# Performance work log

Measured on AMD Instinct MI355X. Metric: run time of the kernel, lower is better.

## Reference

```python
import jax, jax.numpy as jnp
import numpy as np

B, D, K, P = 4096, 510, 128, 332


def setup_inputs() -> dict:
    key = jax.random.key(0)
    k0, k1, k2, k3, k4 = jax.random.split(key, 5)
    z = jax.random.normal(k0, (B, D), dtype=jnp.float32)
    z_pre = jax.random.normal(k1, (B, D), dtype=jnp.float32)
    codebook = jax.random.normal(k2, (K, D), dtype=jnp.float32)
    phrase_table = jax.random.normal(k3, (P, D), dtype=jnp.float32)
    position_number = jax.random.randint(k4, (B,), 0, P, dtype=jnp.int64)
    return {"z": z, "z_pre": z_pre, "codebook": codebook,
            "phrase_table": phrase_table, "position_number": position_number}


def _vq(z, codebook):
    # squared L2 distance via ||z||^2 + ||c||^2 - 2 z.c  (same argmin as tf.norm)
    d2 = (jnp.sum(z * z, axis=-1, keepdims=True)
          + jnp.sum(codebook * codebook, axis=-1)[None, :]
          - 2.0 * jnp.einsum('bd,kd->bk', z, codebook))  # [B, K]
    k = jnp.argmin(d2, axis=-1)                           # [B]
    return codebook[k]                                    # gather -> [B, D]


def reference(z, z_pre, codebook, phrase_table, position_number):
    z_q = _vq(z, codebook)
    z_pre_q = _vq(z_pre, codebook)
    phrase_emb = phrase_table[position_number]            # [B, D]
    combined = z_q + z_pre_q + phrase_emb                 # decoder input in original model
    return combined
```

## Files before the change

kernel.cpp:

```cpp
#include <hip/hip_runtime.h>


#define BHALF 4096
#define D 510
#define K_CODES 128
#define CHB 32768
#define NCHUNK 8
#define WS_NEED (512 + NCHUNK * CHB)

using f32x4  = __attribute__((ext_vector_type(4))) float;
using bf16x8 = __attribute__((ext_vector_type(8))) short;

__device__ __forceinline__ unsigned short f2bf(float f) {
    union { float f; unsigned int u; } v; v.f = f;
    return (unsigned short)((v.u + 0x7FFFu + ((v.u >> 16) & 1u)) >> 16);
}
__device__ __forceinline__ float bf2f(unsigned short h) {
    union { unsigned int u; float f; } v; v.u = ((unsigned int)h) << 16;
    return v.f;
}
__device__ __forceinline__ bool lexlt(float va, int ia, float vb, int ib) {
    return va < vb || (va == vb && ia < ib);
}
#define MFMA16 __builtin_amdgcn_mfma_f32_16x16x32_bf16

__global__ void prep_kernel(const float* __restrict__ cb,
                            float* __restrict__ cnorm,
                            char* __restrict__ img) {
    const int code = blockIdx.x;
    const int l = threadIdx.x;
    const int swz = (code & 7) << 4;
    float s = 0.f;
    #pragma unroll
    for (int i = 0; i < 8; ++i) {
        const int k = l + 64 * i;
        const float v = (k < D) ? cb[(size_t)code * D + k] : 0.f;
        s = fmaf(v, v, s);
        const unsigned short hi = f2bf(v);
        const unsigned short lo = f2bf(v - bf2f(hi));
        char* base = img + (size_t)(k >> 6) * CHB + code * 128;
        const int off = ((k & 63) * 2) ^ swz;
        *(unsigned short*)(base + off) = hi;
        *(unsigned short*)(base + 16384 + off) = lo;
    }
    #pragma unroll
    for (int m = 1; m < 64; m <<= 1) s += __shfl_xor(s, m, 64);
    if (l == 0) cnorm[code] = s;
}

__launch_bounds__(512, 1)
__global__ void main_kernel(const float* __restrict__ z,
                            const float* __restrict__ zp,
                            const float* __restrict__ cb,
                            const float* __restrict__ ph,
                            const int* __restrict__ pos,
                            const float* __restrict__ cnorm,
                            const char* __restrict__ img,
                            float* __restrict__ out) {
    __shared__ __align__(1024) char lds[131072];

    const int tid  = threadIdx.x;
    const int lane = tid & 63;
    const int wu   = __builtin_amdgcn_readfirstlane(tid >> 6);
    const int wn   = wu & 3;
    const int kh   = wu >> 2;
    const int l15  = lane & 15;
    const int kg16 = (lane >> 4) * 16;
    const int r0   = blockIdx.x * 16;

    #pragma unroll
    for (int i = 0; i < 8; ++i) {
        const int u = tid + 512 * i;
        const int row = u >> 7;
        const int col = (u & 127) * 4;
        const float* src = (row < 16) ? z + (size_t)(r0 + row) * D
                                      : zp + (size_t)(r0 + row - 16) * D;
        const float2 va = *(const float2*)(src + col);
        const float2 vb = (col + 2 < D) ? *(const float2*)(src + col + 2)
                                        : make_float2(0.f, 0.f);
        const unsigned short h0 = f2bf(va.x), h1 = f2bf(va.y),
                             h2 = f2bf(vb.x), h3 = f2bf(vb.y);
        const unsigned short g0 = f2bf(va.x - bf2f(h0)), g1 = f2bf(va.y - bf2f(h1)),
                             g2 = f2bf(vb.x - bf2f(h2)), g3 = f2bf(vb.y - bf2f(h3));
        uint2 hi2, lo2;
        hi2.x = (unsigned)h0 | ((unsigned)h1 << 16);
        hi2.y = (unsigned)h2 | ((unsigned)h3 << 16);
        lo2.x = (unsigned)g0 | ((unsigned)g1 << 16);
        lo2.y = (unsigned)g2 | ((unsigned)g3 << 16);
        const int off = row * 1024 + ((col * 2) ^ ((row & 7) << 4));
        *(uint2*)(lds + 65536 + off) = hi2;
        *(uint2*)(lds + 98304 + off) = lo2;
    }
    #pragma unroll
    for (int i = 0; i < 4; ++i) {
        const int u = i * 512 + tid;
        __builtin_amdgcn_global_load_lds(
            (const __attribute__((address_space(1))) void*)(img + (size_t)u * 16),
            (__attribute__((address_space(3))) void*)
                (lds + (size_t)(i * 512 + (tid & ~63)) * 16),
            16, 0, 0);
    }
    __syncthreads();

    f32x4 acc00 = {0.f,0.f,0.f,0.f}, acc01 = {0.f,0.f,0.f,0.f};
    f32x4 acc10 = {0.f,0.f,0.f,0.f}, acc11 = {0.f,0.f,0.f,0.f};

    const int swz = (l15 & 7) << 4;
    const char* zh0 = lds + 65536 + l15 * 1024;
    const char* zl0 = lds + 98304 + l15 * 1024;
    const int code0  = wn * 32 + l15;
    const int cboff0 = code0 * 128;

    int buf = 0;
    for (int c = 0; c < NCHUNK; ++c) {
        if (c < NCHUNK - 1) {
            const char* g = img + (size_t)(c + 1) * CHB;
            #pragma unroll
            for (int i = 0; i < 4; ++i) {
                const int u = i * 512 + tid;
                __builtin_amdgcn_global_load_lds(
                    (const __attribute__((address_space(1))) void*)(g + (size_t)u * 16),
                    (__attribute__((address_space(3))) void*)
                        (lds + (buf ^ 1) * 32768 + (size_t)(i * 512 + (tid & ~63)) * 16),
                    16, 0, 0);
            }
        }
        const int kzB = (c * 128 + kh * 64 + kg16) ^ swz;
        const int kcB = (kh * 64 + kg16) ^ swz;
        const char* cbb = lds + buf * 32768;
        const bf16x8 a0h = *(const bf16x8*)(zh0 + kzB);
        const bf16x8 a0l = *(const bf16x8*)(zl0 + kzB);
        const bf16x8 a1h = *(const bf16x8*)(zh0 + 16384 + kzB);
        const bf16x8 a1l = *(const bf16x8*)(zl0 + 16384 + kzB);
        const bf16x8 b0h = *(const bf16x8*)(cbb + cboff0 + kcB);
        const bf16x8 b0l = *(const bf16x8*)(cbb + 16384 + cboff0 + kcB);
        const bf16x8 b1h = *(const bf16x8*)(cbb + cboff0 + 2048 + kcB);
        const bf16x8 b1l = *(const bf16x8*)(cbb + 16384 + cboff0 + 2048 + kcB);
        acc00 = MFMA16(a0h, b0h, acc00, 0, 0, 0);
        acc01 = MFMA16(a0h, b1h, acc01, 0, 0, 0);
        acc10 = MFMA16(a1h, b0h, acc10, 0, 0, 0);
        acc11 = MFMA16(a1h, b1h, acc11, 0, 0, 0);
        acc00 = MFMA16(a0h, b0l, acc00, 0, 0, 0);
        acc01 = MFMA16(a0h, b1l, acc01, 0, 0, 0);
        acc10 = MFMA16(a1h, b0l, acc10, 0, 0, 0);
        acc11 = MFMA16(a1h, b1l, acc11, 0, 0, 0);
        acc00 = MFMA16(a0l, b0h, acc00, 0, 0, 0);
        acc01 = MFMA16(a0l, b1h, acc01, 0, 0, 0);
        acc10 = MFMA16(a1l, b0h, acc10, 0, 0, 0);
        acc11 = MFMA16(a1l, b1h, acc11, 0, 0, 0);
        __syncthreads();
        buf ^= 1;
    }

    float* ef  = (float*)lds;
    float* tv1 = (float*)(lds + 65536);
    int*   ti1 = (int*)  (lds + 66048);
    float* tv2 = (float*)(lds + 66560);
    int*   ti2 = (int*)  (lds + 67072);
    int*   i1a = (int*)  (lds + 67584);
    int*   i2a = (int*)  (lds + 67712);
    float* refd= (float*)(lds + 67840);
    int*   kbf = (int*)  (lds + 68096);

    if (kh == 1) {
        const int base = wn * 64 + lane;
        #pragma unroll
        for (int j = 0; j < 4; ++j) {
            ef[(0 + j) * 256 + base]  = acc00[j];
            ef[(4 + j) * 256 + base]  = acc01[j];
            ef[(8 + j) * 256 + base]  = acc10[j];
            ef[(12 + j) * 256 + base] = acc11[j];
        }
    }
    __syncthreads();
    if (kh == 0) {
        const int base = wn * 64 + lane;
        #pragma unroll
        for (int j = 0; j < 4; ++j) {
            acc00[j] += ef[(0 + j) * 256 + base];
            acc01[j] += ef[(4 + j) * 256 + base];
            acc10[j] += ef[(8 + j) * 256 + base];
            acc11[j] += ef[(12 + j) * 256 + base];
        }
        const float cn0 = cnorm[code0];
        const float cn1 = cnorm[code0 + 16];
        #pragma unroll
        for (int rf = 0; rf < 2; ++rf) {
            #pragma unroll
            for (int j = 0; j < 4; ++j) {
                const float va = cn0 - 2.f * (rf ? acc10[j] : acc00[j]);
                const float vb = cn1 - 2.f * (rf ? acc11[j] : acc01[j]);
                float v1, v2; int i1, i2;
                if (vb < va) { v1 = vb; i1 = code0 + 16; v2 = va; i2 = code0; }
                else         { v1 = va; i1 = code0;      v2 = vb; i2 = code0 + 16; }
                #pragma unroll
                for (int m = 1; m < 16; m <<= 1) {
                    const float o1 = __shfl_xor(v1, m, 64); const int oi1 = __shfl_xor(i1, m, 64);
                    const float o2 = __shfl_xor(v2, m, 64); const int oi2 = __shfl_xor(i2, m, 64);
                    if (lexlt(o1, oi1, v1, i1)) {
                        if (lexlt(v1, i1, o2, oi2)) { v2 = v1; i2 = i1; }
                        else                        { v2 = o2; i2 = oi2; }
                        v1 = o1; i1 = oi1;
                    } else if (lexlt(o1, oi1, v2, i2)) { v2 = o1; i2 = oi1; }
                }
                if (l15 == 0) {
                    const int mrow = rf * 16 + (lane >> 4) * 4 + j;
                    tv1[wn * 32 + mrow] = v1; ti1[wn * 32 + mrow] = i1;
                    tv2[wn * 32 + mrow] = v2; ti2[wn * 32 + mrow] = i2;
                }
            }
        }
    }
    __syncthreads();

    if (tid < 32) {
        float v1 = tv1[tid]; int i1 = ti1[tid];
        float v2 = tv2[tid]; int i2 = ti2[tid];
        #pragma unroll
        for (int w = 1; w < 4; ++w) {
            const float o1 = tv1[w * 32 + tid], o2 = tv2[w * 32 + tid];
            const int  oi1 = ti1[w * 32 + tid], oi2 = ti2[w * 32 + tid];
            if (lexlt(o1, oi1, v1, i1)) {
                if (lexlt(v1, i1, o2, oi2)) { v2 = v1; i2 = i1; }
                else                        { v2 = o2; i2 = oi2; }
                v1 = o1; i1 = oi1;
            } else if (lexlt(o1, oi1, v2, i2)) { v2 = o1; i2 = oi1; }
        }
        i1a[tid] = i1; i2a[tid] = i2;
    }
    __syncthreads();

    const int grp = tid >> 5, l31 = tid & 31;
    #pragma unroll
    for (int jt = 0; jt < 4; ++jt) {
        const int job = jt * 16 + grp;
        const int row = job >> 1;
        const int cand = (job & 1) ? i2a[row] : i1a[row];
        const float* zr = (row < 16) ? z + (size_t)(r0 + row) * D
                                     : zp + (size_t)(r0 + row - 16) * D;
        const float* cr = cb + (size_t)cand * D;
        float dot = 0.f;
        #pragma unroll
        for (int it = 0; it < 8; ++it) {
            const int col = l31 * 2 + it * 64;
            if (col < D) {
                const float2 a = *(const float2*)(zr + col);
                const float2 b = *(const float2*)(cr + col);
                dot = fmaf(a.x, b.x, fmaf(a.y, b.y, dot));
            }
        }
        #pragma unroll
        for (int m = 1; m < 32; m <<= 1) dot += __shfl_xor(dot, m, 64);
        if (l31 == 0) refd[job] = cnorm[cand] - 2.f * dot;
    }
    __syncthreads();
    if (tid < 32) {
        const float da = refd[tid * 2], db = refd[tid * 2 + 1];
        const int ia = i1a[tid], ib = i2a[tid];
        kbf[tid] = lexlt(db, ib, da, ia) ? ib : ia;
    }
    __syncthreads();

    const int grow = tid >> 5;
    const int kz   = kbf[grow];
    const int kzp2 = kbf[16 + grow];
    const int pp   = pos[r0 + grow];
    const float* ra = cb + (size_t)kz * D;
    const float* rb = cb + (size_t)kzp2 * D;
    const float* rp = ph + (size_t)pp * D;
    float* ro = out + (size_t)(r0 + grow) * D;
    #pragma unroll
    for (int it = 0; it < 8; ++it) {
        const int col = l31 * 2 + it * 64;
        if (col < D) {
            const float2 a = *(const float2*)(ra + col);
            const float2 b = *(const float2*)(rb + col);
            const float2 p = *(const float2*)(rp + col);
            float2 o; o.x = a.x + b.x + p.x; o.y = a.y + b.y + p.y;
            *(float2*)(ro + col) = o;
        }
    }
}

extern "C" void kernel_launch(void* const* d_in, const int* in_sizes, int n_in,
                              void* d_out, int out_size, void* d_ws, size_t ws_size,
                              hipStream_t stream) {
    const float* z  = (const float*)d_in[0];
    const float* zp = (const float*)d_in[1];
    const float* cb = (const float*)d_in[2];
    const float* ph = (const float*)d_in[3];
    const int*   pos = (const int*)d_in[4];
    float* out = (float*)d_out;

    float* cnorm = (float*)d_ws;
    char*  img   = (char*)d_ws + 512;

    prep_kernel<<<K_CODES, 64, 0, stream>>>(cb, cnorm, img);
    main_kernel<<<BHALF / 16, 512, 0, stream>>>(z, zp, cb, ph, pos, cnorm, img, out);
}
```

Measured before the change: 32.64 us.

## Halve rows per block and LDS footprint to raise occupancy and grid size

Each block now handles 8 rows of z and z_pre instead of 16, and uses 64KB of LDS instead of 128KB. This doubles the grid to 512 blocks and allows several blocks per CU. Each wave owns 16 codes across the full K dimension, which removes the cross-wave K-split reduction. The codebook hi/lo image is re-laid out as interleaved 256B rows. Double-buffering of codebook chunks is dropped in favour of one buffer with two barriers per chunk, trading load/compute overlap within a block for overlap across more resident blocks. Every block now re-streams the whole codebook image, so total codebook traffic doubles.

```diff
diff --git a/kernel.cpp b/kernel.cpp
--- a/kernel.cpp
+++ b/kernel.cpp
@@ -6,7 +6,7 @@
 #define K_CODES 128
 #define CHB 32768
 #define NCHUNK 8
-#define WS_NEED (512 + NCHUNK * CHB)
+#define GRID 512
 
 using f32x4  = __attribute__((ext_vector_type(4))) float;
 using bf16x8 = __attribute__((ext_vector_type(8))) short;
@@ -38,17 +38,17 @@
         s = fmaf(v, v, s);
         const unsigned short hi = f2bf(v);
         const unsigned short lo = f2bf(v - bf2f(hi));
-        char* base = img + (size_t)(k >> 6) * CHB + code * 128;
-        const int off = ((k & 63) * 2) ^ swz;
+        char* base = img + (size_t)(k >> 6) * CHB + code * 256;
+        const int off = (((k & 63) * 2) ^ swz);
         *(unsigned short*)(base + off) = hi;
-        *(unsigned short*)(base + 16384 + off) = lo;
+        *(unsigned short*)(base + 128 + off) = lo;
     }
     #pragma unroll
     for (int m = 1; m < 64; m <<= 1) s += __shfl_xor(s, m, 64);
     if (l == 0) cnorm[code] = s;
 }
 
-__launch_bounds__(512, 1)
+__launch_bounds__(512, 4)
 __global__ void main_kernel(const float* __restrict__ z,
                             const float* __restrict__ zp,
                             const float* __restrict__ cb,
@@ -57,24 +57,25 @@
                             const float* __restrict__ cnorm,
                             const char* __restrict__ img,
                             float* __restrict__ out) {
-    __shared__ __align__(1024) char lds[131072];
+    __shared__ __align__(1024) char lds[65536];
 
     const int tid  = threadIdx.x;
     const int lane = tid & 63;
     const int wu   = __builtin_amdgcn_readfirstlane(tid >> 6);
-    const int wn   = wu & 3;
-    const int kh   = wu >> 2;
     const int l15  = lane & 15;
-    const int kg16 = (lane >> 4) * 16;
-    const int r0   = blockIdx.x * 16;
-
-    #pragma unroll
-    for (int i = 0; i < 8; ++i) {
+    const int kq   = lane >> 4;
+    const int r0   = blockIdx.x * 8;
+    const int code = wu * 16 + l15;
+    const int swz  = (l15 & 7) << 4;
+    const float cn0 = cnorm[code];
+
+    #pragma unroll
+    for (int i = 0; i < 4; ++i) {
         const int u = tid + 512 * i;
         const int row = u >> 7;
         const int col = (u & 127) * 4;
-        const float* src = (row < 16) ? z + (size_t)(r0 + row) * D
-                                      : zp + (size_t)(r0 + row - 16) * D;
+        const float* src = (row < 8) ? z + (size_t)(r0 + row) * D
+                                     : zp + (size_t)(r0 + row - 8) * D;
         const float2 va = *(const float2*)(src + col);
         const float2 vb = (col + 2 < D) ? *(const float2*)(src + col + 2)
                                         : make_float2(0.f, 0.f);
@@ -88,161 +89,107 @@
         lo2.x = (unsigned)g0 | ((unsigned)g1 << 16);
         lo2.y = (unsigned)g2 | ((unsigned)g3 << 16);
         const int off = row * 1024 + ((col * 2) ^ ((row & 7) << 4));
-        *(uint2*)(lds + 65536 + off) = hi2;
-        *(uint2*)(lds + 98304 + off) = lo2;
-    }
-    #pragma unroll
-    for (int i = 0; i < 4; ++i) {
-        const int u = i * 512 + tid;
-        __builtin_amdgcn_global_load_lds(
-            (const __attribute__((address_space(1))) void*)(img + (size_t)u * 16),
-            (__attribute__((address_space(3))) void*)
-                (lds + (size_t)(i * 512 + (tid & ~63)) * 16),
-            16, 0, 0);
-    }
-    __syncthreads();
-
-    f32x4 acc00 = {0.f,0.f,0.f,0.f}, acc01 = {0.f,0.f,0.f,0.f};
-    f32x4 acc10 = {0.f,0.f,0.f,0.f}, acc11 = {0.f,0.f,0.f,0.f};
-
-    const int swz = (l15 & 7) << 4;
-    const char* zh0 = lds + 65536 + l15 * 1024;
-    const char* zl0 = lds + 98304 + l15 * 1024;
-    const int code0  = wn * 32 + l15;
-    const int cboff0 = code0 * 128;
-
-    int buf = 0;
+        *(uint2*)(lds + off) = hi2;
+        *(uint2*)(lds + 16384 + off) = lo2;
+    }
+
+    f32x4 acc = {0.f, 0.f, 0.f, 0.f};
+    const char* zh0 = lds + l15 * 1024;
+    const char* zl0 = lds + 16384 + l15 * 1024;
+    const char* cbrow = lds + 32768 + code * 256;
+
     for (int c = 0; c < NCHUNK; ++c) {
-        if (c < NCHUNK - 1) {
-            const char* g = img + (size_t)(c + 1) * CHB;
+        __syncthreads();
+        {
+            const char* g = img + (size_t)c * CHB;
             #pragma unroll
             for (int i = 0; i < 4; ++i) {
                 const int u = i * 512 + tid;
                 __builtin_amdgcn_global_load_lds(
                     (const __attribute__((address_space(1))) void*)(g + (size_t)u * 16),
                     (__attribute__((address_space(3))) void*)
-                        (lds + (buf ^ 1) * 32768 + (size_t)(i * 512 + (tid & ~63)) * 16),
+                        (lds + 32768 + (size_t)(i * 512 + (tid & ~63)) * 16),
                     16, 0, 0);
             }
         }
-        const int kzB = (c * 128 + kh * 64 + kg16) ^ swz;
-        const int kcB = (kh * 64 + kg16) ^ swz;
-        const char* cbb = lds + buf * 32768;
-        const bf16x8 a0h = *(const bf16x8*)(zh0 + kzB);
-        const bf16x8 a0l = *(const bf16x8*)(zl0 + kzB);
-        const bf16x8 a1h = *(const bf16x8*)(zh0 + 16384 + kzB);
-        const bf16x8 a1l = *(const bf16x8*)(zl0 + 16384 + kzB);
-        const bf16x8 b0h = *(const bf16x8*)(cbb + cboff0 + kcB);
-        const bf16x8 b0l = *(const bf16x8*)(cbb + 16384 + cboff0 + kcB);
-        const bf16x8 b1h = *(const bf16x8*)(cbb + cboff0 + 2048 + kcB);
-        const bf16x8 b1l = *(const bf16x8*)(cbb + 16384 + cboff0 + 2048 + kcB);
-        acc00 = MFMA16(a0h, b0h, acc00, 0, 0, 0);
-        acc01 = MFMA16(a0h, b1h, acc01, 0, 0, 0);
-        acc10 = MFMA16(a1h, b0h, acc10, 0, 0, 0);
-        acc11 = MFMA16(a1h, b1h, acc11, 0, 0, 0);
-        acc00 = MFMA16(a0h, b0l, acc00, 0, 0, 0);
-        acc01 = MFMA16(a0h, b1l, acc01, 0, 0, 0);
-        acc10 = MFMA16(a1h, b0l, acc10, 0, 0, 0);
-        acc11 = MFMA16(a1h, b1l, acc11, 0, 0, 0);
-        acc00 = MFMA16(a0l, b0h, acc00, 0, 0, 0);
-        acc01 = MFMA16(a0l, b1h, acc01, 0, 0, 0);
-        acc10 = MFMA16(a1l, b0h, acc10, 0, 0, 0);
-        acc11 = MFMA16(a1l, b1h, acc11, 0, 0, 0);
         __syncthreads();
-        buf ^= 1;
-    }
-
-    float* ef  = (float*)lds;
-    float* tv1 = (float*)(lds + 65536);
-    int*   ti1 = (int*)  (lds + 66048);
-    float* tv2 = (float*)(lds + 66560);
-    int*   ti2 = (int*)  (lds + 67072);
-    int*   i1a = (int*)  (lds + 67584);
-    int*   i2a = (int*)  (lds + 67712);
-    float* refd= (float*)(lds + 67840);
-    int*   kbf = (int*)  (lds + 68096);
-
-    if (kh == 1) {
-        const int base = wn * 64 + lane;
-        #pragma unroll
-        for (int j = 0; j < 4; ++j) {
-            ef[(0 + j) * 256 + base]  = acc00[j];
-            ef[(4 + j) * 256 + base]  = acc01[j];
-            ef[(8 + j) * 256 + base]  = acc10[j];
-            ef[(12 + j) * 256 + base] = acc11[j];
-        }
-    }
-    __syncthreads();
-    if (kh == 0) {
-        const int base = wn * 64 + lane;
-        #pragma unroll
-        for (int j = 0; j < 4; ++j) {
-            acc00[j] += ef[(0 + j) * 256 + base];
-            acc01[j] += ef[(4 + j) * 256 + base];
-            acc10[j] += ef[(8 + j) * 256 + base];
-            acc11[j] += ef[(12 + j) * 256 + base];
-        }
-        const float cn0 = cnorm[code0];
-        const float cn1 = cnorm[code0 + 16];
-        #pragma unroll
-        for (int rf = 0; rf < 2; ++rf) {
-            #pragma unroll
-            for (int j = 0; j < 4; ++j) {
-                const float va = cn0 - 2.f * (rf ? acc10[j] : acc00[j]);
-                const float vb = cn1 - 2.f * (rf ? acc11[j] : acc01[j]);
-                float v1, v2; int i1, i2;
-                if (vb < va) { v1 = vb; i1 = code0 + 16; v2 = va; i2 = code0; }
-                else         { v1 = va; i1 = code0;      v2 = vb; i2 = code0 + 16; }
-                #pragma unroll
-                for (int m = 1; m < 16; m <<= 1) {
-                    const float o1 = __shfl_xor(v1, m, 64); const int oi1 = __shfl_xor(i1, m, 64);
-                    const float o2 = __shfl_xor(v2, m, 64); const int oi2 = __shfl_xor(i2, m, 64);
-                    if (lexlt(o1, oi1, v1, i1)) {
-                        if (lexlt(v1, i1, o2, oi2)) { v2 = v1; i2 = i1; }
-                        else                        { v2 = o2; i2 = oi2; }
-                        v1 = o1; i1 = oi1;
-                    } else if (lexlt(o1, oi1, v2, i2)) { v2 = o1; i2 = oi1; }
-                }
-                if (l15 == 0) {
-                    const int mrow = rf * 16 + (lane >> 4) * 4 + j;
-                    tv1[wn * 32 + mrow] = v1; ti1[wn * 32 + mrow] = i1;
-                    tv2[wn * 32 + mrow] = v2; ti2[wn * 32 + mrow] = i2;
-                }
-            }
-        }
-    }
-    __syncthreads();
-
-    if (tid < 32) {
-        float v1 = tv1[tid]; int i1 = ti1[tid];
-        float v2 = tv2[tid]; int i2 = ti2[tid];
-        #pragma unroll
-        for (int w = 1; w < 4; ++w) {
-            const float o1 = tv1[w * 32 + tid], o2 = tv2[w * 32 + tid];
-            const int  oi1 = ti1[w * 32 + tid], oi2 = ti2[w * 32 + tid];
+        #pragma unroll
+        for (int ks = 0; ks < 2; ++ks) {
+            const int kzB = (c * 128 + ks * 64 + kq * 16) ^ swz;
+            const int kcB = (ks * 64 + kq * 16) ^ swz;
+            const bf16x8 a_h = *(const bf16x8*)(zh0 + kzB);
+            const bf16x8 a_l = *(const bf16x8*)(zl0 + kzB);
+            const bf16x8 b_h = *(const bf16x8*)(cbrow + kcB);
+            const bf16x8 b_l = *(const bf16x8*)(cbrow + 128 + kcB);
+            acc = MFMA16(a_h, b_h, acc, 0, 0, 0);
+            acc = MFMA16(a_h, b_l, acc, 0, 0, 0);
+            acc = MFMA16(a_l, b_h, acc, 0, 0, 0);
+        }
+    }
+    __syncthreads();
+
+    float* tv1 = (float*)(lds);
+    int*   ti1 = (int*)  (lds + 512);
+    float* tv2 = (float*)(lds + 1024);
+    int*   ti2 = (int*)  (lds + 1536);
+    int*   i1a = (int*)  (lds + 2048);
+    int*   i2a = (int*)  (lds + 2112);
+    float* refd= (float*)(lds + 2176);
+    int*   kbf = (int*)  (lds + 2304);
+
+    #pragma unroll
+    for (int j = 0; j < 4; ++j) {
+        float v1 = cn0 - 2.f * acc[j];
+        int   i1 = code;
+        float v2 = 3.4e38f;
+        int   i2 = 1 << 30;
+        #pragma unroll
+        for (int m = 1; m < 16; m <<= 1) {
+            const float o1 = __shfl_xor(v1, m, 64); const int oi1 = __shfl_xor(i1, m, 64);
+            const float o2 = __shfl_xor(v2, m, 64); const int oi2 = __shfl_xor(i2, m, 64);
             if (lexlt(o1, oi1, v1, i1)) {
                 if (lexlt(v1, i1, o2, oi2)) { v2 = v1; i2 = i1; }
                 else                        { v2 = o2; i2 = oi2; }
                 v1 = o1; i1 = oi1;
             } else if (lexlt(o1, oi1, v2, i2)) { v2 = o1; i2 = oi1; }
         }
+        if (l15 == 0) {
+            const int mrow = kq * 4 + j;
+            tv1[wu * 16 + mrow] = v1; ti1[wu * 16 + mrow] = i1;
+            tv2[wu * 16 + mrow] = v2; ti2[wu * 16 + mrow] = i2;
+        }
+    }
+    __syncthreads();
+
+    if (tid < 16) {
+        float v1 = tv1[tid]; int i1 = ti1[tid];
+        float v2 = tv2[tid]; int i2 = ti2[tid];
+        #pragma unroll
+        for (int w = 1; w < 8; ++w) {
+            const float o1 = tv1[w * 16 + tid], o2 = tv2[w * 16 + tid];
+            const int  oi1 = ti1[w * 16 + tid], oi2 = ti2[w * 16 + tid];
+            if (lexlt(o1, oi1, v1, i1)) {
+                if (lexlt(v1, i1, o2, oi2)) { v2 = v1; i2 = i1; }
+                else                        { v2 = o2; i2 = oi2; }
+                v1 = o1; i1 = oi1;
+            } else if (lexlt(o1, oi1, v2, i2)) { v2 = o1; i2 = oi1; }
+        }
         i1a[tid] = i1; i2a[tid] = i2;
     }
     __syncthreads();
 
-    const int grp = tid >> 5, l31 = tid & 31;
-    #pragma unroll
-    for (int jt = 0; jt < 4; ++jt) {
-        const int job = jt * 16 + grp;
+    {
+        const int job = tid >> 4;
+        const int l16 = tid & 15;
         const int row = job >> 1;
         const int cand = (job & 1) ? i2a[row] : i1a[row];
-        const float* zr = (row < 16) ? z + (size_t)(r0 + row) * D
-                                     : zp + (size_t)(r0 + row - 16) * D;
+        const float* zr = (row < 8) ? z + (size_t)(r0 + row) * D
+                                    : zp + (size_t)(r0 + row - 8) * D;
         const float* cr = cb + (size_t)cand * D;
         float dot = 0.f;
         #pragma unroll
-        for (int it = 0; it < 8; ++it) {
-            const int col = l31 * 2 + it * 64;
+        for (int t = 0; t < 16; ++t) {
+            const int col = l16 * 2 + t * 32;
             if (col < D) {
                 const float2 a = *(const float2*)(zr + col);
                 const float2 b = *(const float2*)(cr + col);
@@ -250,34 +197,36 @@
             }
         }
         #pragma unroll
-        for (int m = 1; m < 32; m <<= 1) dot += __shfl_xor(dot, m, 64);
-        if (l31 == 0) refd[job] = cnorm[cand] - 2.f * dot;
-    }
-    __syncthreads();
-    if (tid < 32) {
+        for (int m = 1; m < 16; m <<= 1) dot += __shfl_xor(dot, m, 64);
+        if (l16 == 0) refd[job] = cnorm[cand] - 2.f * dot;
+    }
+    __syncthreads();
+    if (tid < 16) {
         const float da = refd[tid * 2], db = refd[tid * 2 + 1];
         const int ia = i1a[tid], ib = i2a[tid];
         kbf[tid] = lexlt(db, ib, da, ia) ? ib : ia;
     }
     __syncthreads();
 
-    const int grow = tid >> 5;
-    const int kz   = kbf[grow];
-    const int kzp2 = kbf[16 + grow];
-    const int pp   = pos[r0 + grow];
-    const float* ra = cb + (size_t)kz * D;
-    const float* rb = cb + (size_t)kzp2 * D;
-    const float* rp = ph + (size_t)pp * D;
-    float* ro = out + (size_t)(r0 + grow) * D;
-    #pragma unroll
-    for (int it = 0; it < 8; ++it) {
-        const int col = l31 * 2 + it * 64;
-        if (col < D) {
-            const float2 a = *(const float2*)(ra + col);
-            const float2 b = *(const float2*)(rb + col);
-            const float2 p = *(const float2*)(rp + col);
-            float2 o; o.x = a.x + b.x + p.x; o.y = a.y + b.y + p.y;
-            *(float2*)(ro + col) = o;
+    {
+        const int grow = wu;
+        const int kz   = kbf[grow];
+        const int kzp2 = kbf[8 + grow];
+        const int pp   = pos[r0 + grow];
+        const float* ra = cb + (size_t)kz * D;
+        const float* rb = cb + (size_t)kzp2 * D;
+        const float* rp = ph + (size_t)pp * D;
+        float* ro = out + (size_t)(r0 + grow) * D;
+        #pragma unroll
+        for (int q = 0; q < 4; ++q) {
+            const int col = lane * 8 + q * 2;
+            if (col < D) {
+                const float2 a = *(const float2*)(ra + col);
+                const float2 b = *(const float2*)(rb + col);
+                const float2 p = *(const float2*)(rp + col);
+                float2 o; o.x = a.x + b.x + p.x; o.y = a.y + b.y + p.y;
+                *(float2*)(ro + col) = o;
+            }
         }
     }
 }
@@ -296,5 +245,5 @@
     char*  img   = (char*)d_ws + 512;
 
     prep_kernel<<<K_CODES, 64, 0, stream>>>(cb, cnorm, img);
-    main_kernel<<<BHALF / 16, 512, 0, stream>>>(z, zp, cb, ph, pos, cnorm, img, out);
-}
+    main_kernel<<<GRID, 512, 0, stream>>>(z, zp, cb, ph, pos, cnorm, img, out);
+}
```

New measurement: 30.74 us. -5.8%, faster.
